# Optimization experiments

Hardware: AMD Instinct MI355X
Metric: run time of the kernel (lower is better)

Reference implementation:

```python
import jax, jax.numpy as jnp
import numpy as np

DIM = 768
NUM_HEADS = 12
HEAD_DIM = DIM // NUM_HEADS
BASE = 10000.0


def rotate_half(x):
    x1, x2 = jnp.split(x, 2, axis=-1)
    return jnp.concatenate((-x2, x1), axis=-1)


def rope_cos_sin(seq_len, dim, dtype):
    inv_freq = 1.0 / (BASE ** (jnp.arange(0, dim, 2, dtype=jnp.float32) / dim))
    t = jnp.arange(seq_len, dtype=jnp.float32)
    freqs = jnp.einsum('i,j->ij', t, inv_freq)  # [N, dim/2]
    emb = jnp.concatenate((freqs, freqs), axis=-1)  # [N, dim]
    return jnp.cos(emb).astype(dtype), jnp.sin(emb).astype(dtype)


def setup_inputs() -> dict:
    key = jax.random.key(0)
    k1, k2, k3, k4 = jax.random.split(key, 4)
    B, N, C = 1, 4096, DIM
    x = jax.random.normal(k1, (B, N, C), dtype=jnp.float32)
    s = 1.0 / np.sqrt(C)
    qkv_w = jax.random.normal(k2, (3 * C, C), dtype=jnp.float32) * s
    proj_w = jax.random.normal(k3, (C, C), dtype=jnp.float32) * s
    proj_b = jax.random.normal(k4, (C,), dtype=jnp.float32) * 0.01
    return {"x": x, "qkv_w": qkv_w, "proj_w": proj_w, "proj_b": proj_b}


def reference(x, qkv_w, proj_w, proj_b):
    B, N, C = x.shape
    H, D = NUM_HEADS, HEAD_DIM
    scale = D ** -0.5
    qkv = jnp.einsum('bnc,oc->bno', x, qkv_w)           # [B, N, 3C]
    qkv = qkv.reshape(B, N, 3, H, D).transpose(2, 0, 3, 1, 4)  # [3, B, H, N, D]
    q, k, v = qkv[0], qkv[1], qkv[2]
    cos, sin = rope_cos_sin(N, D, x.dtype)              # [N, D] each
    cos = cos[None, None]                               # [1,1,N,D]
    sin = sin[None, None]
    q = q * cos + rotate_half(q) * sin
    k = k * cos + rotate_half(k) * sin
    attn = jnp.einsum('bhqd,bhkd->bhqk', q, k) * scale  # [B,H,N,N]
    attn = jax.nn.softmax(attn, axis=-1)
    out = jnp.einsum('bhqk,bhkd->bhqd', attn, v)        # [B,H,N,D]
    out = out.transpose(0, 2, 1, 3).reshape(B, N, C)
    return jnp.einsum('bnc,oc->bno', out, proj_w) + proj_b
```

## Files before the change

kernel.cpp:

```cpp
#include <hip/hip_runtime.h>
#include <hip/hip_bf16.h>
#include <math.h>

#define DIM 768
#define NHEADS 12
#define HD 64
#define SEQ 4096
#define KSPLIT 4

typedef __bf16 bf16x8 __attribute__((ext_vector_type(8)));
typedef float f32x4 __attribute__((ext_vector_type(4)));

__device__ inline ushort f2bf(float f) {
    union { float f; uint u; } v; v.f = f;
    uint r = v.u + 0x7FFF + ((v.u >> 16) & 1);
    return (ushort)(r >> 16);
}

__global__ __launch_bounds__(256)
void rope_tab_k(float2* __restrict__ tab)
{
    const int idx = blockIdx.x * 256 + threadIdx.x;
    const int j = idx & 31;
    const int n = idx >> 5;
    const float invf = (float)pow(10000.0, -(double)j / 32.0);
    const float ang  = (float)n * invf;
    double s, c;
    sincos((double)ang, &s, &c);
    tab[idx] = make_float2((float)c, (float)s);
}

__global__ __launch_bounds__(256)
void gemm_qkv(const float* __restrict__ A, const float* __restrict__ B,
              const float2* __restrict__ tab,
              ushort* __restrict__ Qb, ushort* __restrict__ Kb,
              ushort* __restrict__ Vp)
{
    constexpr int BM = 128, BN = 128, BK = 64, PAD = 8;
    __shared__ ushort Ah[BM][BK + PAD];
    __shared__ ushort Bh[BN][BK + PAD];

    const int t    = threadIdx.x;
    const int lane = t & 63;
    const int wv   = t >> 6;
    const int wm   = (wv >> 1) * 64;
    const int wn   = (wv & 1) * 64;
    const int m0   = blockIdx.y * BM;
    const int n0   = blockIdx.x * BN;

    f32x4 acc[4][4] = {};

    const int lrow = t >> 4;
    const int lcol = (t & 15) * 4;

    for (int k0 = 0; k0 < DIM; k0 += BK) {
        #pragma unroll
        for (int i = 0; i < 8; ++i) {
            const int row = lrow + i * 16;
            float4 a4 = *(const float4*)&A[(size_t)(m0 + row) * DIM + k0 + lcol];
            float4 b4 = *(const float4*)&B[(size_t)(n0 + row) * DIM + k0 + lcol];
            ushort4 ah, bh;
            ah.x = f2bf(a4.x); ah.y = f2bf(a4.y);
            ah.z = f2bf(a4.z); ah.w = f2bf(a4.w);
            bh.x = f2bf(b4.x); bh.y = f2bf(b4.y);
            bh.z = f2bf(b4.z); bh.w = f2bf(b4.w);
            *(ushort4*)&Ah[row][lcol] = ah;
            *(ushort4*)&Bh[row][lcol] = bh;
        }
        __syncthreads();

        #pragma unroll
        for (int ks = 0; ks < BK; ks += 32) {
            const int koff = ks + ((lane >> 4) << 3);
            const int rs = lane & 15;
            bf16x8 af[4], bf[4];
            #pragma unroll
            for (int i = 0; i < 4; ++i) {
                af[i] = *(const bf16x8*)&Ah[wm + i * 16 + rs][koff];
                bf[i] = *(const bf16x8*)&Bh[wn + i * 16 + rs][koff];
            }
            #pragma unroll
            for (int i = 0; i < 4; ++i)
                #pragma unroll
                for (int j = 0; j < 4; ++j)
                    acc[i][j] = __builtin_amdgcn_mfma_f32_16x16x32_bf16(
                        af[i], bf[j], acc[i][j], 0, 0, 0);
        }
        __syncthreads();
    }

    const int rsel  = lane & 15;
    const int quad  = lane >> 4;
    const int rbase = m0 + wm + (quad << 2);
    const int c0    = n0 + wn;
    const int tt    = c0 / DIM;
    const int h     = (c0 % DIM) >> 6;

    if (tt == 2) {
        const int T = (m0 + wm) >> 6;
        #pragma unroll
        for (int j = 0; j < 4; ++j) {
            const int d = rsel + 16 * j;
            ushort vv[16];
            #pragma unroll
            for (int r = 0; r < 4; ++r)
                #pragma unroll
                for (int i = 0; i < 4; ++i)
                    vv[4 * r + i] = f2bf(acc[i][j][r]);
            ushort* dst = &Vp[((size_t)h * HD + d) * SEQ + T * 64 + 16 * quad];
            *(float4*)&dst[0] = *(const float4*)&vv[0];
            *(float4*)&dst[8] = *(const float4*)&vv[8];
        }
    } else {
        ushort* dstb = (tt == 0 ? Qb : Kb) + (size_t)h * SEQ * HD;
        const float qs = (tt == 0) ? 0.125f : 1.0f;
        #pragma unroll
        for (int i = 0; i < 4; ++i)
            #pragma unroll
            for (int r = 0; r < 4; ++r) {
                const int n = rbase + i * 16 + r;
                #pragma unroll
                for (int j = 0; j < 2; ++j) {
                    const float a = acc[i][j][r];
                    const float b = acc[i][j + 2][r];
                    const float2 cs2 = tab[n * 32 + rsel + 16 * j];
                    dstb[(size_t)n * HD + rsel + 16 * j]      = f2bf((a * cs2.x - b * cs2.y) * qs);
                    dstb[(size_t)n * HD + rsel + 16 * j + 32] = f2bf((b * cs2.x + a * cs2.y) * qs);
                }
            }
    }
}

__global__ __launch_bounds__(256, 4)
void flash_mfma(const ushort* __restrict__ Qb, const ushort* __restrict__ Kb,
                const ushort* __restrict__ Vp,
                float* __restrict__ Opart, float* __restrict__ lpart)
{
    __shared__ ushort Ks[64][68];
    __shared__ ushort Vs[64][68];
    __shared__ ushort Pl[4][32][68];

    const int t    = threadIdx.x;
    const int lane = t & 63;
    const int wv   = t >> 6;
    const int rsel = lane & 15;
    const int quad = lane >> 4;
    const int h    = blockIdx.y;
    const int part = blockIdx.z;
    const int q0   = blockIdx.x * 128 + wv * 32;
    const int Tbeg = (part * (SEQ / KSPLIT)) >> 6;
    const int Tend = Tbeg + (SEQ / KSPLIT) / 64;

    const int crow = t >> 2;
    const int ccol = (t & 3) * 16;

    bf16x8 aq[2][2];
    #pragma unroll
    for (int mi = 0; mi < 2; ++mi)
        #pragma unroll
        for (int ks = 0; ks < 2; ++ks)
            aq[mi][ks] = *(const bf16x8*)&Qb[((size_t)h * SEQ + q0 + 16 * mi + rsel) * HD
                                             + ks * 32 + quad * 8];

    f32x4 accO[2][4] = {};
    float lsum[2][4] = {};

    for (int T = Tbeg; T < Tend; ++T) {
        __syncthreads();
        {
            const ushort* ksrc = &Kb[((size_t)h * SEQ + T * 64 + crow) * HD + ccol];
            *(float4*)&Ks[crow][ccol]     = *(const float4*)&ksrc[0];
            *(float4*)&Ks[crow][ccol + 8] = *(const float4*)&ksrc[8];
            const ushort* vsrc = &Vp[((size_t)h * HD + crow) * SEQ + T * 64 + ccol];
            *(float4*)&Vs[crow][ccol]     = *(const float4*)&vsrc[0];
            *(float4*)&Vs[crow][ccol + 8] = *(const float4*)&vsrc[8];
        }
        __syncthreads();

        bf16x8 bk[4][2];
        #pragma unroll
        for (int n = 0; n < 4; ++n)
            #pragma unroll
            for (int ks = 0; ks < 2; ++ks)
                bk[n][ks] = *(const bf16x8*)&Ks[16 * n + rsel][32 * ks + quad * 8];

        #pragma unroll
        for (int mi = 0; mi < 2; ++mi) {
            f32x4 accS[4] = {};
            #pragma unroll
            for (int ks = 0; ks < 2; ++ks)
                #pragma unroll
                for (int n = 0; n < 4; ++n)
                    accS[n] = __builtin_amdgcn_mfma_f32_16x16x32_bf16(
                        aq[mi][ks], bk[n][ks], accS[n], 0, 0, 0);

            #pragma unroll
            for (int r = 0; r < 4; ++r) {
                const float p0 = __expf(accS[0][r]);
                const float p1 = __expf(accS[1][r]);
                const float p2 = __expf(accS[2][r]);
                const float p3 = __expf(accS[3][r]);
                ushort4 pw;
                pw.x = f2bf(p0); pw.y = f2bf(p1);
                pw.z = f2bf(p2); pw.w = f2bf(p3);
                *(ushort4*)&Pl[wv][16 * mi + 4 * quad + r][4 * rsel] = pw;
                lsum[mi][r] += (p0 + p1) + (p2 + p3);
            }
        }

        asm volatile("s_waitcnt lgkmcnt(0)" ::: "memory");

        bf16x8 bv[4][2];
        #pragma unroll
        for (int j = 0; j < 4; ++j)
            #pragma unroll
            for (int ks = 0; ks < 2; ++ks)
                bv[j][ks] = *(const bf16x8*)&Vs[16 * j + rsel][32 * ks + quad * 8];

        #pragma unroll
        for (int mi = 0; mi < 2; ++mi) {
            bf16x8 ap[2];
            ap[0] = *(const bf16x8*)&Pl[wv][16 * mi + rsel][quad * 8];
            ap[1] = *(const bf16x8*)&Pl[wv][16 * mi + rsel][32 + quad * 8];
            #pragma unroll
            for (int ks = 0; ks < 2; ++ks)
                #pragma unroll
                for (int j = 0; j < 4; ++j)
                    accO[mi][j] = __builtin_amdgcn_mfma_f32_16x16x32_bf16(
                        ap[ks], bv[j][ks], accO[mi][j], 0, 0, 0);
        }
    }

    #pragma unroll
    for (int mi = 0; mi < 2; ++mi)
        #pragma unroll
        for (int r = 0; r < 4; ++r) {
            float s = lsum[mi][r];
            s += __shfl_xor(s, 1);
            s += __shfl_xor(s, 2);
            s += __shfl_xor(s, 4);
            s += __shfl_xor(s, 8);
            lsum[mi][r] = s;
        }

    float* Ob = Opart + ((size_t)part * NHEADS + h) * SEQ * HD;
    float* lb = lpart + ((size_t)part * NHEADS + h) * SEQ;
    #pragma unroll
    for (int mi = 0; mi < 2; ++mi)
        #pragma unroll
        for (int r = 0; r < 4; ++r) {
            const int n = q0 + 16 * mi + 4 * quad + r;
            #pragma unroll
            for (int j = 0; j < 4; ++j)
                Ob[(size_t)n * HD + 16 * j + rsel] = accO[mi][j][r];
            if (rsel == 0) lb[n] = lsum[mi][r];
        }
}

__global__ __launch_bounds__(256)
void merge_k(const float* __restrict__ Opart, const float* __restrict__ lpart,
             ushort* __restrict__ AO)
{
    const int idx = blockIdx.x * 256 + threadIdx.x;
    const int dg = idx & 15;
    const int n  = (idx >> 4) & (SEQ - 1);
    const int h  = idx >> 16;

    float4 o = make_float4(0.f, 0.f, 0.f, 0.f);
    float l = 0.f;
    #pragma unroll
    for (int p = 0; p < KSPLIT; ++p) {
        const float4 v = *(const float4*)&Opart[(((size_t)p * NHEADS + h) * SEQ + n) * HD + dg * 4];
        o.x += v.x; o.y += v.y; o.z += v.z; o.w += v.w;
        l += lpart[((size_t)p * NHEADS + h) * SEQ + n];
    }
    const float inv = 1.f / l;
    ushort4 w;
    w.x = f2bf(o.x * inv); w.y = f2bf(o.y * inv);
    w.z = f2bf(o.z * inv); w.w = f2bf(o.w * inv);
    *(ushort4*)&AO[(size_t)n * DIM + h * HD + dg * 4] = w;
}

__global__ __launch_bounds__(256)
void gemm_proj(const ushort* __restrict__ A, const float* __restrict__ B,
               const float* __restrict__ bias, float* __restrict__ out)
{
    constexpr int BM = 128, BN = 128, BK = 64, PAD = 8;
    __shared__ ushort As[BM][BK + PAD];
    __shared__ ushort Bs[BN][BK + PAD];

    const int t    = threadIdx.x;
    const int lane = t & 63;
    const int wv   = t >> 6;
    const int wm   = (wv >> 1) * 64;
    const int wn   = (wv & 1) * 64;
    const int m0   = blockIdx.y * BM;
    const int n0   = blockIdx.x * BN;

    f32x4 acc[4][4] = {};

    const int arow = t >> 3;
    const int aseg = (t & 7) * 8;
    const int brow = t >> 4;
    const int bcol = (t & 15) * 4;

    for (int k0 = 0; k0 < DIM; k0 += BK) {
        #pragma unroll
        for (int i = 0; i < 4; ++i) {
            const int row = arow + i * 32;
            *(float4*)&As[row][aseg] =
                *(const float4*)&A[(size_t)(m0 + row) * DIM + k0 + aseg];
        }
        #pragma unroll
        for (int i = 0; i < 8; ++i) {
            const int row = brow + i * 16;
            float4 b4 = *(const float4*)&B[(size_t)(n0 + row) * DIM + k0 + bcol];
            ushort4 bh;
            bh.x = f2bf(b4.x); bh.y = f2bf(b4.y);
            bh.z = f2bf(b4.z); bh.w = f2bf(b4.w);
            *(ushort4*)&Bs[row][bcol] = bh;
        }
        __syncthreads();

        #pragma unroll
        for (int ks = 0; ks < BK; ks += 32) {
            const int koff = ks + ((lane >> 4) << 3);
            const int rs = lane & 15;
            bf16x8 af[4], bf[4];
            #pragma unroll
            for (int i = 0; i < 4; ++i) {
                af[i] = *(const bf16x8*)&As[wm + i * 16 + rs][koff];
                bf[i] = *(const bf16x8*)&Bs[wn + i * 16 + rs][koff];
            }
            #pragma unroll
            for (int i = 0; i < 4; ++i)
                #pragma unroll
                for (int j = 0; j < 4; ++j)
                    acc[i][j] = __builtin_amdgcn_mfma_f32_16x16x32_bf16(
                        af[i], bf[j], acc[i][j], 0, 0, 0);
        }
        __syncthreads();
    }

    const int rbase = m0 + wm + ((lane >> 4) << 2);
    const int cbase = n0 + wn + (lane & 15);

    #pragma unroll
    for (int j = 0; j < 4; ++j) {
        const int col = cbase + j * 16;
        const float bv = bias[col];
        #pragma unroll
        for (int i = 0; i < 4; ++i) {
            const int row0 = rbase + i * 16;
            #pragma unroll
            for (int r = 0; r < 4; ++r)
                out[(size_t)(row0 + r) * DIM + col] = acc[i][j][r] + bv;
        }
    }
}

extern "C" void kernel_launch(void* const* d_in, const int* in_sizes, int n_in,
                              void* d_out, int out_size, void* d_ws, size_t ws_size,
                              hipStream_t stream)
{
    const float* x      = (const float*)d_in[0];
    const float* qkv_w  = (const float*)d_in[1];
    const float* proj_w = (const float*)d_in[2];
    const float* proj_b = (const float*)d_in[3];

    const size_t headsz = (size_t)NHEADS * SEQ * HD;
    char* p = (char*)d_ws;
    ushort* Qb    = (ushort*)p;                 p += headsz * 2;
    ushort* Kb    = (ushort*)p;                 p += headsz * 2;
    ushort* Vp    = (ushort*)p;                 p += headsz * 2;
    ushort* AO    = (ushort*)p;                 p += (size_t)SEQ * DIM * 2;
    float*  Opart = (float*)p;                  p += (size_t)KSPLIT * headsz * 4;
    float*  lpart = (float*)p;                  p += (size_t)KSPLIT * NHEADS * SEQ * 4;
    float2* tab   = (float2*)p;
    float*  out   = (float*)d_out;

    rope_tab_k<<<(SEQ * 32) / 256, 256, 0, stream>>>(tab);

    gemm_qkv<<<dim3(3 * DIM / 128, SEQ / 128), 256, 0, stream>>>(
        x, qkv_w, tab, Qb, Kb, Vp);

    flash_mfma<<<dim3(SEQ / 128, NHEADS, KSPLIT), 256, 0, stream>>>(
        Qb, Kb, Vp, Opart, lpart);

    merge_k<<<(NHEADS * SEQ * 16) / 256, 256, 0, stream>>>(Opart, lpart, AO);

    gemm_proj<<<dim3(DIM / 128, SEQ / 128), 256, 0, stream>>>(
        AO, proj_w, proj_b, out);
}
```

Measured before the change: 231.4 us.

## Pre-convert inputs to bf16, shrink P staging, and raise flash occupancy

Adds separate conversion kernels that turn x, qkv_w and proj_w into bf16 before the GEMMs, so the GEMM tile loads read bf16 directly and no longer convert repeatedly per tile. f2bf now uses the hardware bf16 cast. In flash attention, the P staging buffer is halved by handling one 16-row slice at a time, V fragments are loaded alongside K, and the occupancy hint rises from 4 to 6 blocks. In exchange it adds three extra launches and extra memory traffic for the converted copies, and the higher occupancy target may raise register pressure.

```diff
diff --git a/kernel.cpp b/kernel.cpp
--- a/kernel.cpp
+++ b/kernel.cpp
@@ -12,9 +12,20 @@
 typedef float f32x4 __attribute__((ext_vector_type(4)));
 
 __device__ inline ushort f2bf(float f) {
-    union { float f; uint u; } v; v.f = f;
-    uint r = v.u + 0x7FFF + ((v.u >> 16) & 1);
-    return (ushort)(r >> 16);
+    __bf16 b = (__bf16)f;
+    union { __bf16 b; ushort u; } v; v.b = b;
+    return v.u;
+}
+
+__global__ __launch_bounds__(256)
+void cvt_bf16(const float* __restrict__ src, ushort* __restrict__ dst, int n4)
+{
+    const int i = blockIdx.x * 256 + threadIdx.x;
+    if (i >= n4) return;
+    const float4 v = ((const float4*)src)[i];
+    ushort4 w;
+    w.x = f2bf(v.x); w.y = f2bf(v.y); w.z = f2bf(v.z); w.w = f2bf(v.w);
+    ((ushort4*)dst)[i] = w;
 }
 
 __global__ __launch_bounds__(256)
@@ -31,7 +42,7 @@
 }
 
 __global__ __launch_bounds__(256)
-void gemm_qkv(const float* __restrict__ A, const float* __restrict__ B,
+void gemm_qkv(const ushort* __restrict__ A, const ushort* __restrict__ B,
               const float2* __restrict__ tab,
               ushort* __restrict__ Qb, ushort* __restrict__ Kb,
               ushort* __restrict__ Vp)
@@ -50,22 +61,17 @@
 
     f32x4 acc[4][4] = {};
 
-    const int lrow = t >> 4;
-    const int lcol = (t & 15) * 4;
+    const int srow = t >> 3;
+    const int sseg = (t & 7) * 8;
 
     for (int k0 = 0; k0 < DIM; k0 += BK) {
         #pragma unroll
-        for (int i = 0; i < 8; ++i) {
-            const int row = lrow + i * 16;
-            float4 a4 = *(const float4*)&A[(size_t)(m0 + row) * DIM + k0 + lcol];
-            float4 b4 = *(const float4*)&B[(size_t)(n0 + row) * DIM + k0 + lcol];
-            ushort4 ah, bh;
-            ah.x = f2bf(a4.x); ah.y = f2bf(a4.y);
-            ah.z = f2bf(a4.z); ah.w = f2bf(a4.w);
-            bh.x = f2bf(b4.x); bh.y = f2bf(b4.y);
-            bh.z = f2bf(b4.z); bh.w = f2bf(b4.w);
-            *(ushort4*)&Ah[row][lcol] = ah;
-            *(ushort4*)&Bh[row][lcol] = bh;
+        for (int i = 0; i < 4; ++i) {
+            const int row = srow + i * 32;
+            *(float4*)&Ah[row][sseg] =
+                *(const float4*)&A[(size_t)(m0 + row) * DIM + k0 + sseg];
+            *(float4*)&Bh[row][sseg] =
+                *(const float4*)&B[(size_t)(n0 + row) * DIM + k0 + sseg];
         }
         __syncthreads();
 
@@ -131,14 +137,14 @@
     }
 }
 
-__global__ __launch_bounds__(256, 4)
+__global__ __launch_bounds__(256, 6)
 void flash_mfma(const ushort* __restrict__ Qb, const ushort* __restrict__ Kb,
                 const ushort* __restrict__ Vp,
                 float* __restrict__ Opart, float* __restrict__ lpart)
 {
     __shared__ ushort Ks[64][68];
     __shared__ ushort Vs[64][68];
-    __shared__ ushort Pl[4][32][68];
+    __shared__ ushort Pl[4][16][68];
 
     const int t    = threadIdx.x;
     const int lane = t & 63;
@@ -177,12 +183,14 @@
         }
         __syncthreads();
 
-        bf16x8 bk[4][2];
+        bf16x8 bk[4][2], bv[4][2];
         #pragma unroll
         for (int n = 0; n < 4; ++n)
             #pragma unroll
-            for (int ks = 0; ks < 2; ++ks)
+            for (int ks = 0; ks < 2; ++ks) {
                 bk[n][ks] = *(const bf16x8*)&Ks[16 * n + rsel][32 * ks + quad * 8];
+                bv[n][ks] = *(const bf16x8*)&Vs[16 * n + rsel][32 * ks + quad * 8];
+            }
 
         #pragma unroll
         for (int mi = 0; mi < 2; ++mi) {
@@ -203,25 +211,15 @@
                 ushort4 pw;
                 pw.x = f2bf(p0); pw.y = f2bf(p1);
                 pw.z = f2bf(p2); pw.w = f2bf(p3);
-                *(ushort4*)&Pl[wv][16 * mi + 4 * quad + r][4 * rsel] = pw;
+                *(ushort4*)&Pl[wv][4 * quad + r][4 * rsel] = pw;
                 lsum[mi][r] += (p0 + p1) + (p2 + p3);
             }
-        }
-
-        asm volatile("s_waitcnt lgkmcnt(0)" ::: "memory");
-
-        bf16x8 bv[4][2];
-        #pragma unroll
-        for (int j = 0; j < 4; ++j)
-            #pragma unroll
-            for (int ks = 0; ks < 2; ++ks)
-                bv[j][ks] = *(const bf16x8*)&Vs[16 * j + rsel][32 * ks + quad * 8];
-
-        #pragma unroll
-        for (int mi = 0; mi < 2; ++mi) {
+
+            asm volatile("s_waitcnt lgkmcnt(0)" ::: "memory");
+
             bf16x8 ap[2];
-            ap[0] = *(const bf16x8*)&Pl[wv][16 * mi + rsel][quad * 8];
-            ap[1] = *(const bf16x8*)&Pl[wv][16 * mi + rsel][32 + quad * 8];
+            ap[0] = *(const bf16x8*)&Pl[wv][rsel][quad * 8];
+            ap[1] = *(const bf16x8*)&Pl[wv][rsel][32 + quad * 8];
             #pragma unroll
             for (int ks = 0; ks < 2; ++ks)
                 #pragma unroll
@@ -282,7 +280,7 @@
 }
 
 __global__ __launch_bounds__(256)
-void gemm_proj(const ushort* __restrict__ A, const float* __restrict__ B,
+void gemm_proj(const ushort* __restrict__ A, const ushort* __restrict__ B,
                const float* __restrict__ bias, float* __restrict__ out)
 {
     constexpr int BM = 128, BN = 128, BK = 64, PAD = 8;
@@ -299,26 +297,17 @@
 
     f32x4 acc[4][4] = {};
 
-    const int arow = t >> 3;
-    const int aseg = (t & 7) * 8;
-    const int brow = t >> 4;
-    const int bcol = (t & 15) * 4;
+    const int srow = t >> 3;
+    const int sseg = (t & 7) * 8;
 
     for (int k0 = 0; k0 < DIM; k0 += BK) {
         #pragma unroll
         for (int i = 0; i < 4; ++i) {
-            const int row = arow + i * 32;
-            *(float4*)&As[row][aseg] =
-                *(const float4*)&A[(size_t)(m0 + row) * DIM + k0 + aseg];
-        }
-        #pragma unroll
-        for (int i = 0; i < 8; ++i) {
-            const int row = brow + i * 16;
-            float4 b4 = *(const float4*)&B[(size_t)(n0 + row) * DIM + k0 + bcol];
-            ushort4 bh;
-            bh.x = f2bf(b4.x); bh.y = f2bf(b4.y);
-            bh.z = f2bf(b4.z); bh.w = f2bf(b4.w);
-            *(ushort4*)&Bs[row][bcol] = bh;
+            const int row = srow + i * 32;
+            *(float4*)&As[row][sseg] =
+                *(const float4*)&A[(size_t)(m0 + row) * DIM + k0 + sseg];
+            *(float4*)&Bs[row][sseg] =
+                *(const float4*)&B[(size_t)(n0 + row) * DIM + k0 + sseg];
         }
         __syncthreads();
 
@@ -376,13 +365,19 @@
     ushort* AO    = (ushort*)p;                 p += (size_t)SEQ * DIM * 2;
     float*  Opart = (float*)p;                  p += (size_t)KSPLIT * headsz * 4;
     float*  lpart = (float*)p;                  p += (size_t)KSPLIT * NHEADS * SEQ * 4;
-    float2* tab   = (float2*)p;
+    float2* tab   = (float2*)p;                 p += (size_t)SEQ * 32 * sizeof(float2);
+    ushort* xb    = (ushort*)p;                 p += (size_t)SEQ * DIM * 2;
+    ushort* qwb   = (ushort*)p;                 p += (size_t)3 * DIM * DIM * 2;
+    ushort* pwb   = (ushort*)p;
     float*  out   = (float*)d_out;
 
     rope_tab_k<<<(SEQ * 32) / 256, 256, 0, stream>>>(tab);
+    cvt_bf16<<<(SEQ * DIM / 4) / 256, 256, 0, stream>>>(x, xb, SEQ * DIM / 4);
+    cvt_bf16<<<(3 * DIM * DIM / 4) / 256, 256, 0, stream>>>(qkv_w, qwb, 3 * DIM * DIM / 4);
+    cvt_bf16<<<(DIM * DIM / 4) / 256, 256, 0, stream>>>(proj_w, pwb, DIM * DIM / 4);
 
     gemm_qkv<<<dim3(3 * DIM / 128, SEQ / 128), 256, 0, stream>>>(
-        x, qkv_w, tab, Qb, Kb, Vp);
+        xb, qwb, tab, Qb, Kb, Vp);
 
     flash_mfma<<<dim3(SEQ / 128, NHEADS, KSPLIT), 256, 0, stream>>>(
         Qb, Kb, Vp, Opart, lpart);
@@ -390,5 +385,5 @@
     merge_k<<<(NHEADS * SEQ * 16) / 256, 256, 0, stream>>>(Opart, lpart, AO);
 
     gemm_proj<<<dim3(DIM / 128, SEQ / 128), 256, 0, stream>>>(
-        AO, proj_w, proj_b, out);
-}
+        AO, pwb, proj_b, out);
+}
```

Result: slower. 668.3 us (+188.8%).
